# Kernel tuning notes

Measured on AMD Instinct MI355X. Metric: run time of the kernel, lower is better.

The kernel has to match this reference:

```python
import jax, jax.numpy as jnp
import numpy as np
import math

HIDDEN = 1024
NUM_HEADS = 16
HEAD_DIM = HIDDEN // NUM_HEADS
B, S = 4, 1024


def setup_inputs() -> dict:
    key = jax.random.key(0)
    ks = jax.random.split(key, 16)
    sd = 1.0 / math.sqrt(HIDDEN)
    inp = {
        "x": jax.random.normal(ks[0], (B, S, HIDDEN), jnp.float32),
        "spikes": jax.random.uniform(ks[1], (B, S, HIDDEN), jnp.float32),
        "membrane_potential": jax.random.normal(ks[2], (B, S, HIDDEN), jnp.float32),
        "Wq": jax.random.normal(ks[3], (HIDDEN, HIDDEN), jnp.float32) * sd,
        "bq": jnp.zeros((HIDDEN,), jnp.float32),
        "Wk": jax.random.normal(ks[4], (HIDDEN, HIDDEN), jnp.float32) * sd,
        "bk": jnp.zeros((HIDDEN,), jnp.float32),
        "Wv": jax.random.normal(ks[5], (HIDDEN, HIDDEN), jnp.float32) * sd,
        "bv": jnp.zeros((HIDDEN,), jnp.float32),
        "Wo": jax.random.normal(ks[6], (HIDDEN, HIDDEN), jnp.float32) * sd,
        "bo": jnp.zeros((HIDDEN,), jnp.float32),
        "tau_decay": jnp.ones((NUM_HEADS,), jnp.float32) * 10.0,
        "Wg": jax.random.normal(ks[7], (HIDDEN, 2 * HIDDEN), jnp.float32) * sd,
        "bg": jnp.zeros((HIDDEN,), jnp.float32),
    }
    return inp


def _heads(t):  # [B,S,H] -> [B,nH,S,hd]
    Bv, Sv, _ = t.shape
    return t.reshape(Bv, Sv, NUM_HEADS, HEAD_DIM).transpose(0, 2, 1, 3)


def reference(x, spikes, membrane_potential, Wq, bq, Wk, bk, Wv, bv, Wo, bo, tau_decay, Wg, bg):
    scale = 1.0 / math.sqrt(HEAD_DIM)
    q = _heads(x @ Wq.T + bq)
    k = _heads(x @ Wk.T + bk)
    v = _heads(x @ Wv.T + bv)

    # raw scores [B,nH,S,S]
    scores = jnp.einsum('bhqd,bhkd->bhqk', q, k) * scale

    # per-head exponential temporal decay mask [nH,S,S]
    times = jnp.arange(S, dtype=jnp.float32)
    tdiff = jnp.abs(times[:, None] - times[None, :])  # [S,S]
    tmask = jnp.exp(-tdiff[None] / tau_decay[:, None, None])
    scores = scores * tmask[None]

    # spike correlation term
    sm = _heads(spikes)
    spike_attn = jnp.einsum('bhqd,bhkd->bhqk', sm, sm) * scale
    scores = scores * (1.0 + spike_attn)

    # membrane gating of V
    v = v * jax.nn.sigmoid(_heads(membrane_potential))

    probs = jax.nn.softmax(scores, axis=-1)
    context = jnp.einsum('bhqk,bhkd->bhqd', probs, v)
    context = context.transpose(0, 2, 1, 3).reshape(B, S, HIDDEN)

    # dendritic gate
    gate_in = jnp.concatenate([context, membrane_potential], axis=-1)
    gate = jax.nn.sigmoid(gate_in @ Wg.T + bg)
    context = context * gate

    return context @ Wo.T + bo
```

## Files before the change

### kernel.cpp

```cpp
#include <hip/hip_runtime.h>
#include <math.h>
#include <stdint.h>

namespace {

typedef __attribute__((ext_vector_type(8))) short s8v;
typedef __attribute__((ext_vector_type(4))) float f4v;
typedef unsigned short u16;

__device__ __forceinline__ float fexp2(float x) {
  return __builtin_amdgcn_exp2f(x);
}

__device__ __forceinline__ u16 f2bf(float f) {
  union { float f; uint32_t u; } v; v.f = f;
  uint32_t r = v.u + 0x7fffu + ((v.u >> 16) & 1u);
  return (u16)(r >> 16);
}
__device__ __forceinline__ float bf2f(u16 h) {
  union { uint32_t u; float f; } v; v.u = ((uint32_t)h) << 16;
  return v.f;
}
__device__ __forceinline__ uint32_t pk2r(float a, float b) {
  return (uint32_t)f2bf(a) | ((uint32_t)f2bf(b) << 16);
}
__device__ __forceinline__ uint32_t pk2(float a, float b) {
  union { float f; uint32_t u; } x, y; x.f = a; y.f = b;
  return ((x.u + 0x8000u) >> 16) | ((y.u + 0x8000u) & 0xffff0000u);
}
__device__ __forceinline__ float sigmoidf_(float x) { return 1.0f / (1.0f + __expf(-x)); }

__device__ __forceinline__ void gload16(const u16* g, u16* l) {
  __builtin_amdgcn_global_load_lds(
      (const __attribute__((address_space(1))) void*)g,
      (__attribute__((address_space(3))) void*)l, 16, 0, 0);
}

struct CvtJob { const float* src; u16* dst; };
struct CvtArgs { CvtJob j[18]; };

__global__ __launch_bounds__(256) void cvt_kernel(CvtArgs a) {
  const CvtJob jb = a.j[blockIdx.y];
  const int i = blockIdx.x * 256 + threadIdx.x;
  const float4 v = ((const float4*)jb.src)[i];
  uint2 pk;
  pk.x = pk2r(v.x, v.y);
  pk.y = pk2r(v.z, v.w);
  ((uint2*)jb.dst)[i] = pk;
}

__global__ __launch_bounds__(256) void vsum_kernel(
    const u16* __restrict__ Vt, float* __restrict__ Vtot) {
  const int bh = blockIdx.x;
  const int t = threadIdx.x;
  const int d = t >> 2, q = t & 3;
  const uint4* src = (const uint4*)(Vt + ((size_t)bh * 64 + d) * 1024 + q * 256);
  float s = 0.f;
#pragma unroll 8
  for (int i = 0; i < 32; ++i) {
    const uint4 v = src[i];
    s += bf2f((u16)(v.x & 0xffff)) + bf2f((u16)(v.x >> 16));
    s += bf2f((u16)(v.y & 0xffff)) + bf2f((u16)(v.y >> 16));
    s += bf2f((u16)(v.z & 0xffff)) + bf2f((u16)(v.z >> 16));
    s += bf2f((u16)(v.w & 0xffff)) + bf2f((u16)(v.w >> 16));
  }
  s += __shfl_xor(s, 1);
  s += __shfl_xor(s, 2);
  if (q == 0) Vtot[bh * 64 + d] = s;
}

__global__ __launch_bounds__(256) void qkv_gemm(
    const u16* __restrict__ xb,
    const u16* __restrict__ Wqb, const u16* __restrict__ Wkb, const u16* __restrict__ Wvb,
    const float* __restrict__ bq, const float* __restrict__ bk, const float* __restrict__ bv,
    const float* __restrict__ mem,
    u16* __restrict__ Qb, u16* __restrict__ Kb, u16* __restrict__ Vt) {
  __shared__ u16 as_[16384], bs_[16384];
  const int t = threadIdx.x;
  const int nb = blockIdx.x, mb = blockIdx.y;
  const int sel = nb >> 3;
  const u16* W = sel == 0 ? Wqb : (sel == 1 ? Wkb : Wvb);
  const float* bias = sel == 0 ? bq : (sel == 1 ? bk : bv);
  const int m0 = mb * 128, n0 = (nb & 7) * 128;
  const f4v fz = {0.f, 0.f, 0.f, 0.f};
  f4v acc[4][4];
#pragma unroll
  for (int i = 0; i < 4; ++i)
#pragma unroll
    for (int j = 0; j < 4; ++j) acc[i][j] = fz;

  const int l = t & 63, w = t >> 6, wm = w >> 1, wn = w & 1;
  const int lr = l & 15, lq = l >> 4;
  const int rx = lr & 7;
  const int srow = t >> 3;
  const int scol = ((t & 7) ^ (srow & 7)) * 8;

#define QKV_STAGE(k0, bsel)                                                    \
  {                                                                            \
    const int kk_ = (k0);                                                      \
    const int lo_ = (bsel) * 8192;                                             \
    _Pragma("unroll") for (int u = 0; u < 4; ++u) {                            \
      gload16(xb + (size_t)(m0 + u * 32 + srow) * 1024 + kk_ + scol,           \
              as_ + lo_ + u * 2048 + t * 8);                                   \
      gload16(W + (size_t)(n0 + u * 32 + srow) * 1024 + kk_ + scol,            \
              bs_ + lo_ + u * 2048 + t * 8);                                   \
    }                                                                          \
  }

  QKV_STAGE(0, 0);
  int pp = 0;

  if (sel < 2) {
    for (int c = 0; c < 16; ++c) {
      __syncthreads();
      if (c < 15) QKV_STAGE((c + 1) << 6, pp ^ 1);
      const int lo = pp * 8192;
#pragma unroll
      for (int ks = 0; ks < 2; ++ks) {
        const int co = ((ks * 4 + lq) ^ rx) * 8;
        s8v af[4], bf[4];
#pragma unroll
        for (int mi = 0; mi < 4; ++mi)
          af[mi] = *(const s8v*)(as_ + lo + (wm * 64 + mi * 16 + lr) * 64 + co);
#pragma unroll
        for (int ni = 0; ni < 4; ++ni)
          bf[ni] = *(const s8v*)(bs_ + lo + (wn * 64 + ni * 16 + lr) * 64 + co);
#pragma unroll
        for (int mi = 0; mi < 4; ++mi)
#pragma unroll
          for (int ni = 0; ni < 4; ++ni)
            acc[mi][ni] = __builtin_amdgcn_mfma_f32_16x16x32_bf16(
                bf[ni], af[mi], acc[mi][ni], 0, 0, 0);
      }
      pp ^= 1;
    }
    u16* dst = (sel == 0) ? Qb : Kb;
#pragma unroll
    for (int mi = 0; mi < 4; ++mi)
#pragma unroll
      for (int ni = 0; ni < 4; ++ni) {
        const int m = m0 + wm * 64 + mi * 16 + lr;
        const int nb4 = n0 + wn * 64 + ni * 16 + lq * 4;
        const float4 b4 = *(const float4*)&bias[nb4];
        uint2 pk;
        pk.x = pk2r(acc[mi][ni][0] + b4.x, acc[mi][ni][1] + b4.y);
        pk.y = pk2r(acc[mi][ni][2] + b4.z, acc[mi][ni][3] + b4.w);
        *(uint2*)(dst + (size_t)m * 1024 + nb4) = pk;
      }
  } else {
    for (int c = 0; c < 16; ++c) {
      __syncthreads();
      if (c < 15) QKV_STAGE((c + 1) << 6, pp ^ 1);
      const int lo = pp * 8192;
#pragma unroll
      for (int ks = 0; ks < 2; ++ks) {
        const int co = ((ks * 4 + lq) ^ rx) * 8;
        s8v af[4], bf[4];
#pragma unroll
        for (int mi = 0; mi < 4; ++mi)
          af[mi] = *(const s8v*)(as_ + lo + (wm * 64 + mi * 16 + lr) * 64 + co);
#pragma unroll
        for (int ni = 0; ni < 4; ++ni)
          bf[ni] = *(const s8v*)(bs_ + lo + (wn * 64 + ni * 16 + lr) * 64 + co);
#pragma unroll
        for (int mi = 0; mi < 4; ++mi)
#pragma unroll
          for (int ni = 0; ni < 4; ++ni)
            acc[mi][ni] = __builtin_amdgcn_mfma_f32_16x16x32_bf16(
                af[mi], bf[ni], acc[mi][ni], 0, 0, 0);
      }
      pp ^= 1;
    }
    const int b = m0 >> 10;
#pragma unroll
    for (int mi = 0; mi < 4; ++mi)
#pragma unroll
      for (int ni = 0; ni < 4; ++ni) {
        const int mrow = m0 + wm * 64 + mi * 16 + lq * 4;
        const int ncol = n0 + wn * 64 + ni * 16 + lr;
        const int h = ncol >> 6, d = ncol & 63;
        const float bi = bias[ncol];
        float tv[4];
#pragma unroll
        for (int r = 0; r < 4; ++r)
          tv[r] = (acc[mi][ni][r] + bi) * sigmoidf_(mem[(size_t)(mrow + r) * 1024 + ncol]);
        const int s = mrow & 1023;
        uint2 pk;
        pk.x = pk2r(tv[0], tv[1]);
        pk.y = pk2r(tv[2], tv[3]);
        *(uint2*)(Vt + ((size_t)((b * 16 + h) * 64 + d)) * 1024 + s) = pk;
      }
  }
#undef QKV_STAGE
}

template <int MODE>
__global__ __launch_bounds__(256) void gemm64(
    const u16* __restrict__ Ab, const u16* __restrict__ A2b,
    const u16* __restrict__ W, const float* __restrict__ bias,
    u16* __restrict__ outb, float* __restrict__ outf, int K) {
  __shared__ u16 as_[8192], bs_[16384];
  const int t = threadIdx.x, l = t & 63, w = t >> 6;
  const int wm = w >> 1, wn = w & 1, lr = l & 15, lq = l >> 4;
  const int m0 = blockIdx.y * 64, n0 = blockIdx.x * 128;
  const f4v fz = {0.f, 0.f, 0.f, 0.f};
  f4v acc[2][4];
#pragma unroll
  for (int i = 0; i < 2; ++i)
#pragma unroll
    for (int j = 0; j < 4; ++j) acc[i][j] = fz;
  const int rx = lr & 7;
  const int srow = t >> 3;
  const int scol = ((t & 7) ^ (srow & 7)) * 8;
  const int nc = K >> 6;

#define G64_STAGE(k0, bsel)                                                    \
  {                                                                            \
    const int kk_ = (k0);                                                      \
    const u16* Ae_ = Ab;                                                       \
    int ka_ = kk_;                                                             \
    if (MODE == 1 && kk_ >= 1024) { Ae_ = A2b; ka_ = kk_ - 1024; }             \
    _Pragma("unroll") for (int u = 0; u < 2; ++u)                              \
        gload16(Ae_ + (size_t)(m0 + u * 32 + srow) * 1024 + ka_ + scol,        \
                as_ + (bsel) * 4096 + u * 2048 + t * 8);                       \
    _Pragma("unroll") for (int u = 0; u < 4; ++u)                              \
        gload16(W + (size_t)(n0 + u * 32 + srow) * K + kk_ + scol,             \
                bs_ + (bsel) * 8192 + u * 2048 + t * 8);                       \
  }

  G64_STAGE(0, 0);
  int pp = 0;
  for (int c = 0; c < nc; ++c) {
    __syncthreads();
    if (c + 1 < nc) G64_STAGE((c + 1) << 6, pp ^ 1);
    const int loA = pp * 4096, loB = pp * 8192;
#pragma unroll
    for (int ks = 0; ks < 2; ++ks) {
      const int co = ((ks * 4 + lq) ^ rx) * 8;
      s8v af[2], bf[4];
#pragma unroll
      for (int mi = 0; mi < 2; ++mi)
        af[mi] = *(const s8v*)(as_ + loA + (wm * 32 + mi * 16 + lr) * 64 + co);
#pragma unroll
      for (int ni = 0; ni < 4; ++ni)
        bf[ni] = *(const s8v*)(bs_ + loB + (wn * 64 + ni * 16 + lr) * 64 + co);
#pragma unroll
      for (int mi = 0; mi < 2; ++mi)
#pragma unroll
        for (int ni = 0; ni < 4; ++ni)
          acc[mi][ni] = __builtin_amdgcn_mfma_f32_16x16x32_bf16(
              bf[ni], af[mi], acc[mi][ni], 0, 0, 0);
    }
    pp ^= 1;
  }
#undef G64_STAGE

#pragma unroll
  for (int mi = 0; mi < 2; ++mi)
#pragma unroll
    for (int ni = 0; ni < 4; ++ni) {
      const int m = m0 + wm * 32 + mi * 16 + lr;
      const int nb4 = n0 + wn * 64 + ni * 16 + lq * 4;
      const float4 b4 = *(const float4*)&bias[nb4];
      if (MODE == 0) {
        float4 o;
        o.x = acc[mi][ni][0] + b4.x; o.y = acc[mi][ni][1] + b4.y;
        o.z = acc[mi][ni][2] + b4.z; o.w = acc[mi][ni][3] + b4.w;
        *(float4*)(outf + (size_t)m * 1024 + nb4) = o;
      } else {
        const uint2 a2 = *(const uint2*)(Ab + (size_t)m * 1024 + nb4);
        float cx[4] = {bf2f((u16)(a2.x & 0xffff)), bf2f((u16)(a2.x >> 16)),
                       bf2f((u16)(a2.y & 0xffff)), bf2f((u16)(a2.y >> 16))};
        float g[4];
        g[0] = cx[0] * sigmoidf_(acc[mi][ni][0] + b4.x);
        g[1] = cx[1] * sigmoidf_(acc[mi][ni][1] + b4.y);
        g[2] = cx[2] * sigmoidf_(acc[mi][ni][2] + b4.z);
        g[3] = cx[3] * sigmoidf_(acc[mi][ni][3] + b4.w);
        uint2 pk;
        pk.x = pk2r(g[0], g[1]);
        pk.y = pk2r(g[2], g[3]);
        *(uint2*)(outb + (size_t)m * 1024 + nb4) = pk;
      }
    }
}

__global__ __launch_bounds__(256) void attn_mfma(
    const u16* __restrict__ Qb, const u16* __restrict__ Kb,
    const u16* __restrict__ SPb, const u16* __restrict__ Vt,
    const float* __restrict__ tau, const float* __restrict__ Vtot,
    u16* __restrict__ CTXb) {
  __shared__ u16 kbuf[4096], skbuf[4096], vbuf[4096];
  __shared__ u16 pbuf[4][16 * 64];
  const int t = threadIdx.x, l = t & 63, w = t >> 6;
  const int lr = l & 15, lq = l >> 4;
  const int p = blockIdx.x;
  const int g = (p & 7) + 8 * (p >> 7);
  const int qt = (p >> 3) & 15;
  const int h = g & 15, b = g >> 4;

  const float tv_ = tau[h];
  const float c2 = 1.44269504088896f / tv_;
  const float K0 = 0.125f * 1.44269504088896f;
  int rad = (int)ceilf(tv_ * 0.171875f);
  if (rad > 15) rad = 15;
  const int jlo = (qt - rad < 0) ? 0 : qt - rad;
  const int jhi = (qt + rad > 15) ? 15 : qt + rad;
  const int farCnt = 16 - (jhi - jlo + 1);

  float cN[4], cNi[4], cR[4], cRi[4];
#pragma unroll
  for (int i = 0; i < 4; ++i) {
    cN[i]  = fexp2(c2 * (float)(i * 16));
    cNi[i] = fexp2(-c2 * (float)(i * 16));
    cR[i]  = fexp2(c2 * (float)(lq * 4 + i));
    cRi[i] = fexp2(-c2 * (float)(lq * 4 + i));
  }

  s8v qf[2], sf[2];
  {
    const size_t base = ((size_t)(b * 1024 + qt * 64 + w * 16 + lr)) * 1024 + h * 64 + lq * 8;
    qf[0] = *(const s8v*)(Qb + base);
    qf[1] = *(const s8v*)(Qb + base + 32);
    sf[0] = *(const s8v*)(SPb + base);
    sf[1] = *(const s8v*)(SPb + base + 32);
  }
  const s8v ones = {0x3F80, 0x3F80, 0x3F80, 0x3F80, 0x3F80, 0x3F80, 0x3F80, 0x3F80};

  const f4v fz = {0.f, 0.f, 0.f, 0.f};
  f4v oacc[4], vs[4];
  float lacc[4];
#pragma unroll
  for (int i = 0; i < 4; ++i) { oacc[i] = fz; vs[i] = fz; lacc[i] = 0.f; }

  const int iqw = qt * 64 + w * 16;
  const int srow = t >> 3;
  const int csw = ((t & 7) ^ (srow & 7)) * 8;
  const int rx = lr & 7;
  u16* pw = pbuf[w];

  for (int jc = jlo; jc <= jhi; ++jc) {
    const int j0 = jc * 64;
    __syncthreads();
    {
      const size_t kg = ((size_t)(b * 1024 + j0 + srow)) * 1024 + h * 64 + csw;
      gload16(Kb + kg, kbuf + t * 8);
      gload16(Kb + kg + 32 * 1024, kbuf + 2048 + t * 8);
      gload16(SPb + kg, skbuf + t * 8);
      gload16(SPb + kg + 32 * 1024, skbuf + 2048 + t * 8);
      const size_t vg = ((size_t)((b * 16 + h) * 64 + srow)) * 1024 + j0 + csw;
      gload16(Vt + vg, vbuf + t * 8);
      gload16(Vt + vg + 32 * 1024, vbuf + 2048 + t * 8);
    }
    __syncthreads();

    f4v sa[4], ssa[4];
#pragma unroll
    for (int ni = 0; ni < 4; ++ni) { sa[ni] = fz; ssa[ni] = fz; }
#pragma unroll
    for (int ks = 0; ks < 2; ++ks) {
#pragma unroll
      for (int ni = 0; ni < 4; ++ni) {
        const int off = (ni * 16 + lr) * 64 + (((ks * 4 + lq) ^ rx) * 8);
        const s8v kf = *(const s8v*)(kbuf + off);
        sa[ni] = __builtin_amdgcn_mfma_f32_16x16x32_bf16(kf, qf[ks], sa[ni], 0, 0, 0);
        const s8v skf = *(const s8v*)(skbuf + off);
        ssa[ni] = __builtin_amdgcn_mfma_f32_16x16x32_bf16(skf, sf[ks], ssa[ni], 0, 0, 0);
      }
    }

    const int D0 = iqw - j0;
    float pv[4][4];
    if (jc < qt) {
      const float EA = K0 * fexp2(-c2 * (float)(D0 + lr));
#pragma unroll
      for (int ni = 0; ni < 4; ++ni)
#pragma unroll
        for (int r = 0; r < 4; ++r) {
          const float t1 = fmaf(ssa[ni][r], 0.125f, 1.0f);
          const float sc2 = sa[ni][r] * cN[ni] * cR[r] * EA * t1;
          const float e = fexp2(sc2);
          pv[ni][r] = e;
          lacc[ni] += e;
        }
    } else if (jc > qt) {
      const float EAi = K0 * fexp2(c2 * (float)(D0 + lr));
#pragma unroll
      for (int ni = 0; ni < 4; ++ni)
#pragma unroll
        for (int r = 0; r < 4; ++r) {
          const float t1 = fmaf(ssa[ni][r], 0.125f, 1.0f);
          const float sc2 = sa[ni][r] * cNi[ni] * cRi[r] * EAi * t1;
          const float e = fexp2(sc2);
          pv[ni][r] = e;
          lacc[ni] += e;
        }
    } else {
      const float EA  = K0 * fexp2(-c2 * (float)(D0 + lr));
      const float EAi = K0 * fexp2(c2 * (float)(D0 + lr));
#pragma unroll
      for (int ni = 0; ni < 4; ++ni)
#pragma unroll
        for (int r = 0; r < 4; ++r) {
          const int jloc = ni * 16 + lq * 4 + r;
          const float fb = cN[ni] * cR[r] * EA;
          const float fa = cNi[ni] * cRi[r] * EAi;
          const float f = (D0 + lr >= jloc) ? fb : fa;
          const float t1 = fmaf(ssa[ni][r], 0.125f, 1.0f);
          const float e = fexp2(sa[ni][r] * f * t1);
          pv[ni][r] = e;
          lacc[ni] += e;
        }
    }

#pragma unroll
    for (int ni = 0; ni < 4; ++ni) {
      const int phys = (ni * 2 + (lq >> 1)) ^ rx;
      uint2 p2;
      p2.x = pk2(pv[ni][0], pv[ni][1]);
      p2.y = pk2(pv[ni][2], pv[ni][3]);
      *(uint2*)(pw + lr * 64 + phys * 8 + (lq & 1) * 4) = p2;
    }

#pragma unroll
    for (int ks = 0; ks < 2; ++ks) {
      const s8v pf = *(const s8v*)(pw + lr * 64 + (((ks * 4 + lq) ^ rx) * 8));
#pragma unroll
      for (int nd = 0; nd < 4; ++nd) {
        const int off = (nd * 16 + lr) * 64 + (((ks * 4 + lq) ^ rx) * 8);
        const s8v vf = *(const s8v*)(vbuf + off);
        oacc[nd] = __builtin_amdgcn_mfma_f32_16x16x32_bf16(vf, pf, oacc[nd], 0, 0, 0);
        vs[nd] = __builtin_amdgcn_mfma_f32_16x16x32_bf16(vf, ones, vs[nd], 0, 0, 0);
      }
    }
  }

  float ls = (lacc[0] + lacc[1]) + (lacc[2] + lacc[3]);
  ls += __shfl_xor(ls, 16);
  ls += __shfl_xor(ls, 32);
  ls += 64.0f * (float)farCnt;
  const float inv = 1.0f / ls;
  const float* vt0 = Vtot + (size_t)(b * 16 + h) * 64;
  const size_t orow = ((size_t)(b * 1024 + qt * 64 + w * 16 + lr)) * 1024 + h * 64;
#pragma unroll
  for (int nd = 0; nd < 4; ++nd) {
    const float4 vt4 = *(const float4*)(vt0 + nd * 16 + lq * 4);
    float o0 = (oacc[nd][0] + vt4.x - vs[nd][0]) * inv;
    float o1 = (oacc[nd][1] + vt4.y - vs[nd][1]) * inv;
    float o2 = (oacc[nd][2] + vt4.z - vs[nd][2]) * inv;
    float o3 = (oacc[nd][3] + vt4.w - vs[nd][3]) * inv;
    uint2 o;
    o.x = pk2r(o0, o1);
    o.y = pk2r(o2, o3);
    *(uint2*)(CTXb + orow + nd * 16 + lq * 4) = o;
  }
}

}

extern "C" void kernel_launch(void* const* d_in, const int* in_sizes, int n_in,
                              void* d_out, int out_size, void* d_ws, size_t ws_size,
                              hipStream_t stream) {
  const float* x      = (const float*)d_in[0];
  const float* spikes = (const float*)d_in[1];
  const float* mem    = (const float*)d_in[2];
  const float* Wq     = (const float*)d_in[3];
  const float* bq     = (const float*)d_in[4];
  const float* Wk     = (const float*)d_in[5];
  const float* bk     = (const float*)d_in[6];
  const float* Wv     = (const float*)d_in[7];
  const float* bv     = (const float*)d_in[8];
  const float* Wo     = (const float*)d_in[9];
  const float* bo     = (const float*)d_in[10];
  const float* tau    = (const float*)d_in[11];
  const float* Wg     = (const float*)d_in[12];
  const float* bg     = (const float*)d_in[13];
  float* out = (float*)d_out;

  uint8_t* w8 = (uint8_t*)d_ws;
  u16* spb  = (u16*)(w8);
  u16* xb   = (u16*)(w8 + (8u << 20));
  u16* Wqb  = (u16*)(w8 + (16u << 20));
  u16* Wkb  = (u16*)(w8 + (18u << 20));
  u16* Wvb  = (u16*)(w8 + (20u << 20));
  u16* Wob  = (u16*)(w8 + (22u << 20));
  u16* Wgb  = (u16*)(w8 + (24u << 20));
  u16* Qb   = (u16*)(w8 + (28u << 20));
  u16* Kb   = (u16*)(w8 + (36u << 20));
  u16* Vt   = (u16*)(w8 + (44u << 20));
  u16* CTXb = (u16*)(w8 + (52u << 20));
  float* Vtot = (float*)(w8 + (60u << 20));
  u16* memb = (u16*)d_out;
  u16* gctx = xb;

  constexpr size_t QE = 262144 * 4;
  CvtArgs ca;
  for (int q = 0; q < 4; ++q) ca.j[q]     = {x + q * QE,      xb + q * QE};
  for (int q = 0; q < 4; ++q) ca.j[4 + q] = {spikes + q * QE, spb + q * QE};
  for (int q = 0; q < 4; ++q) ca.j[8 + q] = {mem + q * QE,    memb + q * QE};
  ca.j[12] = {Wq, Wqb};
  ca.j[13] = {Wk, Wkb};
  ca.j[14] = {Wv, Wvb};
  ca.j[15] = {Wo, Wob};
  ca.j[16] = {Wg, Wgb};
  ca.j[17] = {Wg + QE, Wgb + QE};
  cvt_kernel<<<dim3(1024, 18), 256, 0, stream>>>(ca);

  qkv_gemm<<<dim3(24, 32), 256, 0, stream>>>(xb, Wqb, Wkb, Wvb, bq, bk, bv, mem,
                                             Qb, Kb, Vt);
  vsum_kernel<<<dim3(64), 256, 0, stream>>>(Vt, Vtot);
  attn_mfma<<<dim3(1024), 256, 0, stream>>>(Qb, Kb, spb, Vt, tau, Vtot, CTXb);
  gemm64<1><<<dim3(8, 64), 256, 0, stream>>>(CTXb, memb, Wgb, bg, gctx, nullptr, 2048);
  gemm64<0><<<dim3(8, 64), 256, 0, stream>>>(gctx, nullptr, Wob, bo, nullptr, out, 1024);
}
```

Measured before the change: 263.2 us.

## Load GEMM fragments directly from global memory and fuse V column-sum via atomics

The QKV and the two projection GEMMs stop staging tiles through LDS with global_load_lds and barriers. Each wave now loads its MFMA fragments straight from global memory into registers, double-buffered, with fully unrolled K loops and a launch bound of two blocks. The separate vsum kernel is removed: the V epilogue accumulates per-column partial sums and atomically adds them into Vtot, which the conversion kernel zeroes first. This removes LDS traffic, barriers and one kernel launch, but it loses reuse of operands across waves, so more global/L2 reads are issued and register pressure rises. The atomics also make the Vtot summation order nondeterministic.

```diff
diff --git a/kernel.cpp b/kernel.cpp
--- a/kernel.cpp
+++ b/kernel.cpp
@@ -37,9 +37,13 @@
 }
 
 struct CvtJob { const float* src; u16* dst; };
-struct CvtArgs { CvtJob j[18]; };
+struct CvtArgs { CvtJob j[18]; float* vz; };
 
 __global__ __launch_bounds__(256) void cvt_kernel(CvtArgs a) {
+  if (blockIdx.y == 0 && blockIdx.x < 4) {
+    float4 z; z.x = 0.f; z.y = 0.f; z.z = 0.f; z.w = 0.f;
+    ((float4*)a.vz)[blockIdx.x * 256 + threadIdx.x] = z;
+  }
   const CvtJob jb = a.j[blockIdx.y];
   const int i = blockIdx.x * 256 + threadIdx.x;
   const float4 v = ((const float4*)jb.src)[i];
@@ -49,33 +53,13 @@
   ((uint2*)jb.dst)[i] = pk;
 }
 
-__global__ __launch_bounds__(256) void vsum_kernel(
-    const u16* __restrict__ Vt, float* __restrict__ Vtot) {
-  const int bh = blockIdx.x;
-  const int t = threadIdx.x;
-  const int d = t >> 2, q = t & 3;
-  const uint4* src = (const uint4*)(Vt + ((size_t)bh * 64 + d) * 1024 + q * 256);
-  float s = 0.f;
-#pragma unroll 8
-  for (int i = 0; i < 32; ++i) {
-    const uint4 v = src[i];
-    s += bf2f((u16)(v.x & 0xffff)) + bf2f((u16)(v.x >> 16));
-    s += bf2f((u16)(v.y & 0xffff)) + bf2f((u16)(v.y >> 16));
-    s += bf2f((u16)(v.z & 0xffff)) + bf2f((u16)(v.z >> 16));
-    s += bf2f((u16)(v.w & 0xffff)) + bf2f((u16)(v.w >> 16));
-  }
-  s += __shfl_xor(s, 1);
-  s += __shfl_xor(s, 2);
-  if (q == 0) Vtot[bh * 64 + d] = s;
-}
-
-__global__ __launch_bounds__(256) void qkv_gemm(
+__global__ __launch_bounds__(256, 2) void qkv_gemm(
     const u16* __restrict__ xb,
     const u16* __restrict__ Wqb, const u16* __restrict__ Wkb, const u16* __restrict__ Wvb,
     const float* __restrict__ bq, const float* __restrict__ bk, const float* __restrict__ bv,
     const float* __restrict__ mem,
-    u16* __restrict__ Qb, u16* __restrict__ Kb, u16* __restrict__ Vt) {
-  __shared__ u16 as_[16384], bs_[16384];
+    u16* __restrict__ Qb, u16* __restrict__ Kb, u16* __restrict__ Vt,
+    float* __restrict__ Vtot) {
   const int t = threadIdx.x;
   const int nb = blockIdx.x, mb = blockIdx.y;
   const int sel = nb >> 3;
@@ -91,48 +75,34 @@
 
   const int l = t & 63, w = t >> 6, wm = w >> 1, wn = w & 1;
   const int lr = l & 15, lq = l >> 4;
-  const int rx = lr & 7;
-  const int srow = t >> 3;
-  const int scol = ((t & 7) ^ (srow & 7)) * 8;
-
-#define QKV_STAGE(k0, bsel)                                                    \
-  {                                                                            \
-    const int kk_ = (k0);                                                      \
-    const int lo_ = (bsel) * 8192;                                             \
-    _Pragma("unroll") for (int u = 0; u < 4; ++u) {                            \
-      gload16(xb + (size_t)(m0 + u * 32 + srow) * 1024 + kk_ + scol,           \
-              as_ + lo_ + u * 2048 + t * 8);                                   \
-      gload16(W + (size_t)(n0 + u * 32 + srow) * 1024 + kk_ + scol,            \
-              bs_ + lo_ + u * 2048 + t * 8);                                   \
-    }                                                                          \
-  }
-
-  QKV_STAGE(0, 0);
-  int pp = 0;
+
+  const u16* Ap = xb + (size_t)(m0 + wm * 64 + lr) * 1024 + lq * 8;
+  const u16* Bp = W + (size_t)(n0 + wn * 64 + lr) * 1024 + lq * 8;
+
+  s8v afb[2][2][4], bfb[2][2][4];
+
+#define QLOAD(bsel, c)                                                         \
+  _Pragma("unroll") for (int ks_ = 0; ks_ < 2; ++ks_)                          \
+  _Pragma("unroll") for (int i2 = 0; i2 < 4; ++i2) {                           \
+    afb[bsel][ks_][i2] = *(const s8v*)(Ap + i2 * 16384 + (c) * 64 + ks_ * 32); \
+    bfb[bsel][ks_][i2] = *(const s8v*)(Bp + i2 * 16384 + (c) * 64 + ks_ * 32); \
+  }
+
+  QLOAD(0, 0);
 
   if (sel < 2) {
+#pragma unroll
     for (int c = 0; c < 16; ++c) {
-      __syncthreads();
-      if (c < 15) QKV_STAGE((c + 1) << 6, pp ^ 1);
-      const int lo = pp * 8192;
-#pragma unroll
-      for (int ks = 0; ks < 2; ++ks) {
-        const int co = ((ks * 4 + lq) ^ rx) * 8;
-        s8v af[4], bf[4];
-#pragma unroll
-        for (int mi = 0; mi < 4; ++mi)
-          af[mi] = *(const s8v*)(as_ + lo + (wm * 64 + mi * 16 + lr) * 64 + co);
-#pragma unroll
-        for (int ni = 0; ni < 4; ++ni)
-          bf[ni] = *(const s8v*)(bs_ + lo + (wn * 64 + ni * 16 + lr) * 64 + co);
+      const int cur = c & 1;
+      if (c < 15) { QLOAD(cur ^ 1, c + 1); }
+#pragma unroll
+      for (int ks = 0; ks < 2; ++ks)
 #pragma unroll
         for (int mi = 0; mi < 4; ++mi)
 #pragma unroll
           for (int ni = 0; ni < 4; ++ni)
             acc[mi][ni] = __builtin_amdgcn_mfma_f32_16x16x32_bf16(
-                bf[ni], af[mi], acc[mi][ni], 0, 0, 0);
-      }
-      pp ^= 1;
+                bfb[cur][ks][ni], afb[cur][ks][mi], acc[mi][ni], 0, 0, 0);
     }
     u16* dst = (sel == 0) ? Qb : Kb;
 #pragma unroll
@@ -148,30 +118,21 @@
         *(uint2*)(dst + (size_t)m * 1024 + nb4) = pk;
       }
   } else {
+#pragma unroll
     for (int c = 0; c < 16; ++c) {
-      __syncthreads();
-      if (c < 15) QKV_STAGE((c + 1) << 6, pp ^ 1);
-      const int lo = pp * 8192;
-#pragma unroll
-      for (int ks = 0; ks < 2; ++ks) {
-        const int co = ((ks * 4 + lq) ^ rx) * 8;
-        s8v af[4], bf[4];
-#pragma unroll
-        for (int mi = 0; mi < 4; ++mi)
-          af[mi] = *(const s8v*)(as_ + lo + (wm * 64 + mi * 16 + lr) * 64 + co);
-#pragma unroll
-        for (int ni = 0; ni < 4; ++ni)
-          bf[ni] = *(const s8v*)(bs_ + lo + (wn * 64 + ni * 16 + lr) * 64 + co);
+      const int cur = c & 1;
+      if (c < 15) { QLOAD(cur ^ 1, c + 1); }
+#pragma unroll
+      for (int ks = 0; ks < 2; ++ks)
 #pragma unroll
         for (int mi = 0; mi < 4; ++mi)
 #pragma unroll
           for (int ni = 0; ni < 4; ++ni)
             acc[mi][ni] = __builtin_amdgcn_mfma_f32_16x16x32_bf16(
-                af[mi], bf[ni], acc[mi][ni], 0, 0, 0);
-      }
-      pp ^= 1;
+                afb[cur][ks][mi], bfb[cur][ks][ni], acc[mi][ni], 0, 0, 0);
     }
     const int b = m0 >> 10;
+    float vpart[4] = {0.f, 0.f, 0.f, 0.f};
 #pragma unroll
     for (int mi = 0; mi < 4; ++mi)
 #pragma unroll
@@ -184,22 +145,28 @@
 #pragma unroll
         for (int r = 0; r < 4; ++r)
           tv[r] = (acc[mi][ni][r] + bi) * sigmoidf_(mem[(size_t)(mrow + r) * 1024 + ncol]);
+        vpart[ni] += (tv[0] + tv[1]) + (tv[2] + tv[3]);
         const int s = mrow & 1023;
         uint2 pk;
         pk.x = pk2r(tv[0], tv[1]);
         pk.y = pk2r(tv[2], tv[3]);
         *(uint2*)(Vt + ((size_t)((b * 16 + h) * 64 + d)) * 1024 + s) = pk;
       }
-  }
-#undef QKV_STAGE
-}
-
-template <int MODE>
-__global__ __launch_bounds__(256) void gemm64(
+#pragma unroll
+    for (int ni = 0; ni < 4; ++ni) {
+      const int ncol = n0 + wn * 64 + ni * 16 + lr;
+      atomicAdd(&Vtot[(size_t)(b * 16 + (ncol >> 6)) * 64 + (ncol & 63)], vpart[ni]);
+    }
+  }
+#undef QLOAD
+}
+
+template <int MODE, int NC>
+__global__ __launch_bounds__(256, 2) void gemm64(
     const u16* __restrict__ Ab, const u16* __restrict__ A2b,
     const u16* __restrict__ W, const float* __restrict__ bias,
-    u16* __restrict__ outb, float* __restrict__ outf, int K) {
-  __shared__ u16 as_[8192], bs_[16384];
+    u16* __restrict__ outb, float* __restrict__ outf) {
+  constexpr int K = NC * 64;
   const int t = threadIdx.x, l = t & 63, w = t >> 6;
   const int wm = w >> 1, wn = w & 1, lr = l & 15, lq = l >> 4;
   const int m0 = blockIdx.y * 64, n0 = blockIdx.x * 128;
@@ -209,51 +176,43 @@
   for (int i = 0; i < 2; ++i)
 #pragma unroll
     for (int j = 0; j < 4; ++j) acc[i][j] = fz;
-  const int rx = lr & 7;
-  const int srow = t >> 3;
-  const int scol = ((t & 7) ^ (srow & 7)) * 8;
-  const int nc = K >> 6;
-
-#define G64_STAGE(k0, bsel)                                                    \
+
+  const u16* Apt = Ab + (size_t)(m0 + wm * 32 + lr) * 1024 + lq * 8;
+  const u16* A2pt = (MODE == 1)
+      ? A2b + (size_t)(m0 + wm * 32 + lr) * 1024 + lq * 8 : Apt;
+  const u16* Bpt = W + (size_t)(n0 + wn * 64 + lr) * K + lq * 8;
+
+  s8v afb[2][2][2], bfb[2][2][4];
+
+#define GLOAD(bsel, c)                                                         \
   {                                                                            \
-    const int kk_ = (k0);                                                      \
-    const u16* Ae_ = Ab;                                                       \
-    int ka_ = kk_;                                                             \
-    if (MODE == 1 && kk_ >= 1024) { Ae_ = A2b; ka_ = kk_ - 1024; }             \
-    _Pragma("unroll") for (int u = 0; u < 2; ++u)                              \
-        gload16(Ae_ + (size_t)(m0 + u * 32 + srow) * 1024 + ka_ + scol,        \
-                as_ + (bsel) * 4096 + u * 2048 + t * 8);                       \
-    _Pragma("unroll") for (int u = 0; u < 4; ++u)                              \
-        gload16(W + (size_t)(n0 + u * 32 + srow) * K + kk_ + scol,             \
-                bs_ + (bsel) * 8192 + u * 2048 + t * 8);                       \
-  }
-
-  G64_STAGE(0, 0);
-  int pp = 0;
-  for (int c = 0; c < nc; ++c) {
-    __syncthreads();
-    if (c + 1 < nc) G64_STAGE((c + 1) << 6, pp ^ 1);
-    const int loA = pp * 4096, loB = pp * 8192;
-#pragma unroll
-    for (int ks = 0; ks < 2; ++ks) {
-      const int co = ((ks * 4 + lq) ^ rx) * 8;
-      s8v af[2], bf[4];
-#pragma unroll
-      for (int mi = 0; mi < 2; ++mi)
-        af[mi] = *(const s8v*)(as_ + loA + (wm * 32 + mi * 16 + lr) * 64 + co);
-#pragma unroll
-      for (int ni = 0; ni < 4; ++ni)
-        bf[ni] = *(const s8v*)(bs_ + loB + (wn * 64 + ni * 16 + lr) * 64 + co);
+    const int kk_ = (c) * 64;                                                  \
+    const u16* Ae_ = (MODE == 1 && kk_ >= 1024) ? A2pt + (kk_ - 1024)          \
+                                                : Apt + kk_;                   \
+    _Pragma("unroll") for (int ks_ = 0; ks_ < 2; ++ks_) {                      \
+      _Pragma("unroll") for (int i2 = 0; i2 < 2; ++i2)                         \
+        afb[bsel][ks_][i2] = *(const s8v*)(Ae_ + i2 * 16384 + ks_ * 32);       \
+      _Pragma("unroll") for (int i2 = 0; i2 < 4; ++i2)                         \
+        bfb[bsel][ks_][i2] =                                                   \
+            *(const s8v*)(Bpt + (size_t)i2 * 16 * K + kk_ + ks_ * 32);         \
+    }                                                                          \
+  }
+
+  GLOAD(0, 0);
+#pragma unroll
+  for (int c = 0; c < NC; ++c) {
+    const int cur = c & 1;
+    if (c + 1 < NC) { GLOAD(cur ^ 1, c + 1); }
+#pragma unroll
+    for (int ks = 0; ks < 2; ++ks)
 #pragma unroll
       for (int mi = 0; mi < 2; ++mi)
 #pragma unroll
         for (int ni = 0; ni < 4; ++ni)
           acc[mi][ni] = __builtin_amdgcn_mfma_f32_16x16x32_bf16(
-              bf[ni], af[mi], acc[mi][ni], 0, 0, 0);
-    }
-    pp ^= 1;
-  }
-#undef G64_STAGE
+              bfb[cur][ks][ni], afb[cur][ks][mi], acc[mi][ni], 0, 0, 0);
+  }
+#undef GLOAD
 
 #pragma unroll
   for (int mi = 0; mi < 2; ++mi)
@@ -377,8 +336,7 @@
 #pragma unroll
         for (int r = 0; r < 4; ++r) {
           const float t1 = fmaf(ssa[ni][r], 0.125f, 1.0f);
-          const float sc2 = sa[ni][r] * cN[ni] * cR[r] * EA * t1;
-          const float e = fexp2(sc2);
+          const float e = fexp2(sa[ni][r] * cN[ni] * cR[r] * EA * t1);
           pv[ni][r] = e;
           lacc[ni] += e;
         }
@@ -389,8 +347,7 @@
 #pragma unroll
         for (int r = 0; r < 4; ++r) {
           const float t1 = fmaf(ssa[ni][r], 0.125f, 1.0f);
-          const float sc2 = sa[ni][r] * cNi[ni] * cRi[r] * EAi * t1;
-          const float e = fexp2(sc2);
+          const float e = fexp2(sa[ni][r] * cNi[ni] * cRi[r] * EAi * t1);
           pv[ni][r] = e;
           lacc[ni] += e;
         }
@@ -503,12 +460,12 @@
   ca.j[15] = {Wo, Wob};
   ca.j[16] = {Wg, Wgb};
   ca.j[17] = {Wg + QE, Wgb + QE};
+  ca.vz = Vtot;
   cvt_kernel<<<dim3(1024, 18), 256, 0, stream>>>(ca);
 
   qkv_gemm<<<dim3(24, 32), 256, 0, stream>>>(xb, Wqb, Wkb, Wvb, bq, bk, bv, mem,
-                                             Qb, Kb, Vt);
-  vsum_kernel<<<dim3(64), 256, 0, stream>>>(Vt, Vtot);
+                                             Qb, Kb, Vt, Vtot);
   attn_mfma<<<dim3(1024), 256, 0, stream>>>(Qb, Kb, spb, Vt, tau, Vtot, CTXb);
-  gemm64<1><<<dim3(8, 64), 256, 0, stream>>>(CTXb, memb, Wgb, bg, gctx, nullptr, 2048);
-  gemm64<0><<<dim3(8, 64), 256, 0, stream>>>(gctx, nullptr, Wob, bo, nullptr, out, 1024);
-}
+  gemm64<1, 32><<<dim3(8, 64), 256, 0, stream>>>(CTXb, memb, Wgb, bg, gctx, nullptr);
+  gemm64<0, 16><<<dim3(8, 64), 256, 0, stream>>>(gctx, nullptr, Wob, bo, nullptr, out);
+}
```

New measurement: 407.3 us. +54.8%, slower.

## Fold V column sums into QKV GEMM epilogue and single-buffer its LDS

Applied to the files above, without the earlier changes.

Removes the separate vsum kernel. The per-(batch,head,dim) V sums are now accumulated in the QKV GEMM epilogue with atomicAdd, and the accumulator is zeroed inside the conversion kernel. The QKV GEMM also switches from double-buffered to single-buffered LDS: fragments are read into registers, then a barrier, then the next tile's global-to-LDS load is issued before the MFMAs. This halves LDS use, which may raise occupancy, at the cost of an extra barrier per k-step and adds float atomics whose summation order is nondeterministic.

```diff
diff --git a/kernel.cpp b/kernel.cpp
--- a/kernel.cpp
+++ b/kernel.cpp
@@ -37,9 +37,13 @@
 }
 
 struct CvtJob { const float* src; u16* dst; };
-struct CvtArgs { CvtJob j[18]; };
+struct CvtArgs { CvtJob j[18]; float* vz; };
 
 __global__ __launch_bounds__(256) void cvt_kernel(CvtArgs a) {
+  if (blockIdx.y == 0 && blockIdx.x < 4) {
+    float4 z; z.x = 0.f; z.y = 0.f; z.z = 0.f; z.w = 0.f;
+    ((float4*)a.vz)[blockIdx.x * 256 + threadIdx.x] = z;
+  }
   const CvtJob jb = a.j[blockIdx.y];
   const int i = blockIdx.x * 256 + threadIdx.x;
   const float4 v = ((const float4*)jb.src)[i];
@@ -49,33 +53,14 @@
   ((uint2*)jb.dst)[i] = pk;
 }
 
-__global__ __launch_bounds__(256) void vsum_kernel(
-    const u16* __restrict__ Vt, float* __restrict__ Vtot) {
-  const int bh = blockIdx.x;
-  const int t = threadIdx.x;
-  const int d = t >> 2, q = t & 3;
-  const uint4* src = (const uint4*)(Vt + ((size_t)bh * 64 + d) * 1024 + q * 256);
-  float s = 0.f;
-#pragma unroll 8
-  for (int i = 0; i < 32; ++i) {
-    const uint4 v = src[i];
-    s += bf2f((u16)(v.x & 0xffff)) + bf2f((u16)(v.x >> 16));
-    s += bf2f((u16)(v.y & 0xffff)) + bf2f((u16)(v.y >> 16));
-    s += bf2f((u16)(v.z & 0xffff)) + bf2f((u16)(v.z >> 16));
-    s += bf2f((u16)(v.w & 0xffff)) + bf2f((u16)(v.w >> 16));
-  }
-  s += __shfl_xor(s, 1);
-  s += __shfl_xor(s, 2);
-  if (q == 0) Vtot[bh * 64 + d] = s;
-}
-
 __global__ __launch_bounds__(256) void qkv_gemm(
     const u16* __restrict__ xb,
     const u16* __restrict__ Wqb, const u16* __restrict__ Wkb, const u16* __restrict__ Wvb,
     const float* __restrict__ bq, const float* __restrict__ bk, const float* __restrict__ bv,
     const float* __restrict__ mem,
-    u16* __restrict__ Qb, u16* __restrict__ Kb, u16* __restrict__ Vt) {
-  __shared__ u16 as_[16384], bs_[16384];
+    u16* __restrict__ Qb, u16* __restrict__ Kb, u16* __restrict__ Vt,
+    float* __restrict__ Vtot) {
+  __shared__ u16 as_[8192], bs_[8192];
   const int t = threadIdx.x;
   const int nb = blockIdx.x, mb = blockIdx.y;
   const int sel = nb >> 3;
@@ -95,44 +80,43 @@
   const int srow = t >> 3;
   const int scol = ((t & 7) ^ (srow & 7)) * 8;
 
-#define QKV_STAGE(k0, bsel)                                                    \
+#define QKV_STAGE(k0)                                                          \
   {                                                                            \
     const int kk_ = (k0);                                                      \
-    const int lo_ = (bsel) * 8192;                                             \
     _Pragma("unroll") for (int u = 0; u < 4; ++u) {                            \
       gload16(xb + (size_t)(m0 + u * 32 + srow) * 1024 + kk_ + scol,           \
-              as_ + lo_ + u * 2048 + t * 8);                                   \
+              as_ + u * 2048 + t * 8);                                         \
       gload16(W + (size_t)(n0 + u * 32 + srow) * 1024 + kk_ + scol,            \
-              bs_ + lo_ + u * 2048 + t * 8);                                   \
+              bs_ + u * 2048 + t * 8);                                         \
     }                                                                          \
   }
 
-  QKV_STAGE(0, 0);
-  int pp = 0;
+  QKV_STAGE(0);
 
   if (sel < 2) {
     for (int c = 0; c < 16; ++c) {
       __syncthreads();
-      if (c < 15) QKV_STAGE((c + 1) << 6, pp ^ 1);
-      const int lo = pp * 8192;
+      s8v af[2][4], bf[2][4];
 #pragma unroll
       for (int ks = 0; ks < 2; ++ks) {
         const int co = ((ks * 4 + lq) ^ rx) * 8;
-        s8v af[4], bf[4];
 #pragma unroll
         for (int mi = 0; mi < 4; ++mi)
-          af[mi] = *(const s8v*)(as_ + lo + (wm * 64 + mi * 16 + lr) * 64 + co);
+          af[ks][mi] = *(const s8v*)(as_ + (wm * 64 + mi * 16 + lr) * 64 + co);
 #pragma unroll
         for (int ni = 0; ni < 4; ++ni)
-          bf[ni] = *(const s8v*)(bs_ + lo + (wn * 64 + ni * 16 + lr) * 64 + co);
+          bf[ks][ni] = *(const s8v*)(bs_ + (wn * 64 + ni * 16 + lr) * 64 + co);
+      }
+      __syncthreads();
+      if (c < 15) QKV_STAGE((c + 1) << 6);
+#pragma unroll
+      for (int ks = 0; ks < 2; ++ks)
 #pragma unroll
         for (int mi = 0; mi < 4; ++mi)
 #pragma unroll
           for (int ni = 0; ni < 4; ++ni)
             acc[mi][ni] = __builtin_amdgcn_mfma_f32_16x16x32_bf16(
-                bf[ni], af[mi], acc[mi][ni], 0, 0, 0);
-      }
-      pp ^= 1;
+                bf[ks][ni], af[ks][mi], acc[mi][ni], 0, 0, 0);
     }
     u16* dst = (sel == 0) ? Qb : Kb;
 #pragma unroll
@@ -150,28 +134,30 @@
   } else {
     for (int c = 0; c < 16; ++c) {
       __syncthreads();
-      if (c < 15) QKV_STAGE((c + 1) << 6, pp ^ 1);
-      const int lo = pp * 8192;
+      s8v af[2][4], bf[2][4];
 #pragma unroll
       for (int ks = 0; ks < 2; ++ks) {
         const int co = ((ks * 4 + lq) ^ rx) * 8;
-        s8v af[4], bf[4];
 #pragma unroll
         for (int mi = 0; mi < 4; ++mi)
-          af[mi] = *(const s8v*)(as_ + lo + (wm * 64 + mi * 16 + lr) * 64 + co);
+          af[ks][mi] = *(const s8v*)(as_ + (wm * 64 + mi * 16 + lr) * 64 + co);
 #pragma unroll
         for (int ni = 0; ni < 4; ++ni)
-          bf[ni] = *(const s8v*)(bs_ + lo + (wn * 64 + ni * 16 + lr) * 64 + co);
+          bf[ks][ni] = *(const s8v*)(bs_ + (wn * 64 + ni * 16 + lr) * 64 + co);
+      }
+      __syncthreads();
+      if (c < 15) QKV_STAGE((c + 1) << 6);
+#pragma unroll
+      for (int ks = 0; ks < 2; ++ks)
 #pragma unroll
         for (int mi = 0; mi < 4; ++mi)
 #pragma unroll
           for (int ni = 0; ni < 4; ++ni)
             acc[mi][ni] = __builtin_amdgcn_mfma_f32_16x16x32_bf16(
-                af[mi], bf[ni], acc[mi][ni], 0, 0, 0);
-      }
-      pp ^= 1;
+                af[ks][mi], bf[ks][ni], acc[mi][ni], 0, 0, 0);
     }
     const int b = m0 >> 10;
+    float vpart[4] = {0.f, 0.f, 0.f, 0.f};
 #pragma unroll
     for (int mi = 0; mi < 4; ++mi)
 #pragma unroll
@@ -184,12 +170,18 @@
 #pragma unroll
         for (int r = 0; r < 4; ++r)
           tv[r] = (acc[mi][ni][r] + bi) * sigmoidf_(mem[(size_t)(mrow + r) * 1024 + ncol]);
+        vpart[ni] += (tv[0] + tv[1]) + (tv[2] + tv[3]);
         const int s = mrow & 1023;
         uint2 pk;
         pk.x = pk2r(tv[0], tv[1]);
         pk.y = pk2r(tv[2], tv[3]);
         *(uint2*)(Vt + ((size_t)((b * 16 + h) * 64 + d)) * 1024 + s) = pk;
       }
+#pragma unroll
+    for (int ni = 0; ni < 4; ++ni) {
+      const int ncol = n0 + wn * 64 + ni * 16 + lr;
+      atomicAdd(&Vtot[(size_t)(b * 16 + (ncol >> 6)) * 64 + (ncol & 63)], vpart[ni]);
+    }
   }
 #undef QKV_STAGE
 }
@@ -377,8 +369,7 @@
 #pragma unroll
         for (int r = 0; r < 4; ++r) {
           const float t1 = fmaf(ssa[ni][r], 0.125f, 1.0f);
-          const float sc2 = sa[ni][r] * cN[ni] * cR[r] * EA * t1;
-          const float e = fexp2(sc2);
+          const float e = fexp2(sa[ni][r] * cN[ni] * cR[r] * EA * t1);
           pv[ni][r] = e;
           lacc[ni] += e;
         }
@@ -389,8 +380,7 @@
 #pragma unroll
         for (int r = 0; r < 4; ++r) {
           const float t1 = fmaf(ssa[ni][r], 0.125f, 1.0f);
-          const float sc2 = sa[ni][r] * cNi[ni] * cRi[r] * EAi * t1;
-          const float e = fexp2(sc2);
+          const float e = fexp2(sa[ni][r] * cNi[ni] * cRi[r] * EAi * t1);
           pv[ni][r] = e;
           lacc[ni] += e;
         }
@@ -503,11 +493,11 @@
   ca.j[15] = {Wo, Wob};
   ca.j[16] = {Wg, Wgb};
   ca.j[17] = {Wg + QE, Wgb + QE};
+  ca.vz = Vtot;
   cvt_kernel<<<dim3(1024, 18), 256, 0, stream>>>(ca);
 
   qkv_gemm<<<dim3(24, 32), 256, 0, stream>>>(xb, Wqb, Wkb, Wvb, bq, bk, bv, mem,
-                                             Qb, Kb, Vt);
-  vsum_kernel<<<dim3(64), 256, 0, stream>>>(Vt, Vtot);
+                                             Qb, Kb, Vt, Vtot);
   attn_mfma<<<dim3(1024), 256, 0, stream>>>(Qb, Kb, spb, Vt, tau, Vtot, CTXb);
   gemm64<1><<<dim3(8, 64), 256, 0, stream>>>(CTXb, memb, Wgb, bg, gctx, nullptr, 2048);
   gemm64<0><<<dim3(8, 64), 256, 0, stream>>>(gctx, nullptr, Wob, bo, nullptr, out, 1024);
```

New measurement: 259.5 us. No clear change (-1.4%).
